# Optimization experiments

Hardware: AMD Instinct MI355X
Metric: run time of the kernel (lower is better)

Reference implementation:

```python
import jax, jax.numpy as jnp
import numpy as np

N_EXPERTS, D_MODEL, D_FF, TOP_K, N_TOKENS = 8, 1024, 4096, 2, 8192

def _uniform_init(key, shape, fan_in):
    # matches torch init: gain = sqrt(1/3), std = gain/sqrt(fan_in), bound = sqrt(3)*std
    bound = np.sqrt(3.0) * np.sqrt(1.0 / 3.0) / np.sqrt(fan_in)
    return jax.random.uniform(key, shape, minval=-bound, maxval=bound, dtype=jnp.float32)

def setup_inputs() -> dict:
    key = jax.random.key(0)
    kx, ki, kw, k1, k2, k3 = jax.random.split(key, 6)
    x = jax.random.normal(kx, (N_TOKENS, D_MODEL), dtype=jnp.float32)
    expert_indices = jax.random.randint(ki, (N_TOKENS, TOP_K), 0, N_EXPERTS, dtype=jnp.int32)
    expert_weights = jax.random.uniform(kw, (N_TOKENS, TOP_K), dtype=jnp.float32)
    w1 = _uniform_init(k1, (N_EXPERTS, D_MODEL, D_FF), D_MODEL)
    w2 = _uniform_init(k2, (N_EXPERTS, D_MODEL, D_FF), D_MODEL)
    w3 = _uniform_init(k3, (N_EXPERTS, D_FF, D_MODEL), D_FF)
    return {"x": x, "expert_indices": expert_indices, "expert_weights": expert_weights,
            "w1": w1, "w2": w2, "w3": w3}

def reference(x, expert_indices, expert_weights, w1, w2, w3):
    # For each token t and routed expert e with routing weight p:
    #   out[t] += p * (silu(x[t] @ W1[e]) * (x[t] @ W2[e])) @ W3[e]
    # Loop over the small fixed expert set; compute each expert's SwiGLU FFN
    # densely over all tokens and combine with per-token routing weights
    # (mathematically identical to the sorted-dispatch grouped GEMM).
    n_experts = w1.shape[0]
    out = jnp.zeros_like(x)
    for e in range(n_experts):
        gate = x @ w1[e]                 # [N, d_ff]
        val = x @ w2[e]                  # [N, d_ff]
        y = (jax.nn.silu(gate) * val) @ w3[e]   # [N, d_model]
        # sum routing weights over top_k slots that picked expert e
        p = jnp.sum(jnp.where(expert_indices == e, expert_weights, 0.0), axis=1)
        out = out + p[:, None] * y
    return out
```

## Files before the change

### kernel.cpp

```cpp
#include <hip/hip_runtime.h>
#include <hip/hip_bf16.h>

typedef __attribute__((ext_vector_type(8))) short short8;
typedef __attribute__((ext_vector_type(4))) float f32x4;
typedef unsigned short u16;
typedef unsigned int u32;

#define NTOK   8192
#define DMODEL 1024
#define DFF    4096
#define NEXP   8
#define NPAIR  (NTOK * 2)
#define PADM   256
#define MT1    72
#define PPAD   (MT1 * PADM)

#define OFF_XB   0ull
#define OFF_W1T  (OFF_XB  + (size_t)NTOK * DMODEL * 2)
#define OFF_W2T  (OFF_W1T + (size_t)NEXP * DFF * DMODEL * 2)
#define OFF_W3T  (OFF_W2T + (size_t)NEXP * DFF * DMODEL * 2)
#define OFF_H    (OFF_W3T + (size_t)NEXP * DMODEL * DFF * 2)
#define OFF_TOK  (OFF_H   + (size_t)PPAD * DFF * 2)
#define OFF_WGT  (OFF_TOK + (size_t)PPAD * 4)
#define OFF_CNT  (OFF_WGT + (size_t)PPAD * 4)
#define OFF_CUR  (OFF_CNT + 64)
#define OFF_OFFP (OFF_CUR + 64)
#define WS_END   (OFF_OFFP + 64)

#define GLOAD16(gp, lp)                                                        \
  __builtin_amdgcn_global_load_lds(                                            \
      (const __attribute__((address_space(1))) u32*)(gp),                      \
      (__attribute__((address_space(3))) u32*)(lp), 16, 0, 0)

__device__ __forceinline__ u16 f2bu(float f) {
  __hip_bfloat16 b = __float2bfloat16(f);
  return __builtin_bit_cast(u16, b);
}


__global__ __launch_bounds__(256) void cvt_x_k(const float* __restrict__ x,
                                               u16* __restrict__ xb) {
  int i = blockIdx.x * 256 + threadIdx.x;
  float4 v = ((const float4*)x)[i];
  unsigned long long pk = (unsigned long long)f2bu(v.x) |
                          ((unsigned long long)f2bu(v.y) << 16) |
                          ((unsigned long long)f2bu(v.z) << 32) |
                          ((unsigned long long)f2bu(v.w) << 48);
  ((unsigned long long*)xb)[i] = pk;
}

__global__ __launch_bounds__(256) void tr_cvt_k(const float* __restrict__ src,
                                                u16* __restrict__ dst, int R, int C) {
  src += (size_t)blockIdx.z * R * C;
  dst += (size_t)blockIdx.z * R * C;
  const int c0 = blockIdx.x * 64, r0 = blockIdx.y * 128;
  __shared__ u16 t[128][68];
  const int tid = threadIdx.x;
  const int cl = (tid & 15) * 4, rl = tid >> 4;
#pragma unroll
  for (int p = 0; p < 8; ++p) {
    int r = rl + p * 16;
    float4 v = *(const float4*)(src + (size_t)(r0 + r) * C + c0 + cl);
    unsigned long long pk = (unsigned long long)f2bu(v.x) |
                            ((unsigned long long)f2bu(v.y) << 16) |
                            ((unsigned long long)f2bu(v.z) << 32) |
                            ((unsigned long long)f2bu(v.w) << 48);
    *(unsigned long long*)&t[r][cl] = pk;
  }
  __syncthreads();
  const int c = tid >> 2, seg = tid & 3;
#pragma unroll
  for (int s = 0; s < 4; ++s) {
    int rbase = (s * 4 + seg) * 8;
    short8 o;
#pragma unroll
    for (int j = 0; j < 8; ++j) o[j] = (short)t[rbase + j][c];
    *(short8*)(dst + (size_t)(c0 + c) * R + r0 + rbase) = o;
  }
}


__global__ __launch_bounds__(256) void count_k(const int* __restrict__ ei,
                                               int* __restrict__ cnt) {
  int i = blockIdx.x * 256 + threadIdx.x;
  atomicAdd(&cnt[ei[i]], 1);
}

__global__ void scan_k(const int* __restrict__ cnt, int* __restrict__ offp) {
  if (threadIdx.x == 0) {
    int a = 0;
#pragma unroll
    for (int e = 0; e < NEXP; ++e) { offp[e] = a; a += (cnt[e] + PADM - 1) & ~(PADM - 1); }
    offp[NEXP] = a;
  }
}

__global__ __launch_bounds__(256) void scatter_k(const int* __restrict__ ei,
                                                 const float* __restrict__ ew,
                                                 const int* __restrict__ offp,
                                                 int* __restrict__ cur,
                                                 int* __restrict__ tok,
                                                 float* __restrict__ wg) {
  int i = blockIdx.x * 256 + threadIdx.x;
  int e = ei[i];
  int p = offp[e] + atomicAdd(&cur[e], 1);
  tok[p] = i >> 1;
  wg[p] = ew[i];
}


#define S1_BUF 16384
#define S1_NK  32

__global__ __launch_bounds__(512, 2) void stage1_k(const u16* __restrict__ xb,
                                                   const u16* __restrict__ w1t,
                                                   const u16* __restrict__ w2t,
                                                   u16* __restrict__ h,
                                                   const int* __restrict__ tok,
                                                   const int* __restrict__ offp) {
  extern __shared__ __align__(16) u16 lds[];
  const int r0 = blockIdx.y * PADM;
  if (r0 >= offp[NEXP]) return;
  int e = 0;
#pragma unroll
  for (int q = 0; q < 7; ++q) e += (offp[e + 1] <= r0) ? 1 : 0;
  const int n0 = blockIdx.x * 128;
  const int tid = threadIdx.x;
  const int lane = tid & 63, w = tid >> 6;
  const int wm = w >> 2, wn = w & 3;

  const int sl = lane & 3, rl = lane >> 2;
  const u16* aga[2];
  int adb[2];
#pragma unroll
  for (int j = 0; j < 2; ++j) {
    int row = w * 32 + j * 16 + rl;
    int t = tok[r0 + row];
    aga[j] = xb + (size_t)t * DMODEL + ((sl ^ ((row >> 1) & 3)) << 3);
    adb[j] = (w * 32 + j * 16) * 32;
  }
  const u16* w1e = w1t + (size_t)e * DFF * DMODEL;
  const u16* w2e = w2t + (size_t)e * DFF * DMODEL;
  const u16* bg1; const u16* bg2;
  int bdb;
  {
    int row = w * 16 + rl;
    size_t ro = (size_t)(n0 + row) * DMODEL + ((sl ^ ((row >> 1) & 3)) << 3);
    bg1 = w1e + ro; bg2 = w2e + ro;
    bdb = (w * 16) * 32;
  }

  int aoff[8], boff[2];
  {
    int ks = lane >> 4;
#pragma unroll
    for (int mi = 0; mi < 8; ++mi) {
      int row = wm * 128 + mi * 16 + (lane & 15);
      aoff[mi] = row * 32 + ((ks ^ ((row >> 1) & 3)) << 3);
    }
#pragma unroll
    for (int ni = 0; ni < 2; ++ni) {
      int col = wn * 32 + ni * 16 + (lane & 15);
      boff[ni] = col * 32 + ((ks ^ ((col >> 1) & 3)) << 3);
    }
  }

  f32x4 accg[8][2], accv[8][2];
  const f32x4 zero = {0.f, 0.f, 0.f, 0.f};
#pragma unroll
  for (int mi = 0; mi < 8; ++mi)
#pragma unroll
    for (int ni = 0; ni < 2; ++ni) { accg[mi][ni] = zero; accv[mi][ni] = zero; }

#define S1_ISSUE(Q, KO)                                                        \
  do {                                                                         \
    GLOAD16(aga[0] + (KO), (Q) + adb[0]);                                      \
    GLOAD16(aga[1] + (KO), (Q) + adb[1]);                                      \
    GLOAD16(bg1 + (KO), (Q) + 8192 + bdb);                                     \
    GLOAD16(bg2 + (KO), (Q) + 12288 + bdb);                                    \
  } while (0)

  S1_ISSUE(lds, 0);
  S1_ISSUE(lds + S1_BUF, 32);
  asm volatile("s_waitcnt vmcnt(4)" ::: "memory");
  __builtin_amdgcn_s_barrier();
  __builtin_amdgcn_sched_barrier(0);

#define S1_STEP(P, KC, ISSUE)                                                  \
  {                                                                            \
    const u16* Ab  = lds + (P) * S1_BUF;                                       \
    const u16* B1b = Ab + 8192;                                                \
    const u16* B2b = Ab + 12288;                                               \
    short8 af[8], b1f[2], b2f[2];                                              \
    _Pragma("unroll") for (int mi = 0; mi < 8; ++mi)                           \
      af[mi] = *(const short8*)(Ab + aoff[mi]);                                \
    _Pragma("unroll") for (int ni = 0; ni < 2; ++ni) {                         \
      b1f[ni] = *(const short8*)(B1b + boff[ni]);                              \
      b2f[ni] = *(const short8*)(B2b + boff[ni]);                              \
    }                                                                          \
    if (ISSUE) S1_ISSUE(lds + (((P) + 2) % 3) * S1_BUF, ((KC) + 2) * 32);      \
    __builtin_amdgcn_s_setprio(1);                                             \
    _Pragma("unroll") for (int mi = 0; mi < 8; ++mi)                           \
      _Pragma("unroll") for (int ni = 0; ni < 2; ++ni) {                       \
        accg[mi][ni] = __builtin_amdgcn_mfma_f32_16x16x32_bf16(                \
            af[mi], b1f[ni], accg[mi][ni], 0, 0, 0);                           \
        accv[mi][ni] = __builtin_amdgcn_mfma_f32_16x16x32_bf16(                \
            af[mi], b2f[ni], accv[mi][ni], 0, 0, 0);                           \
      }                                                                        \
    __builtin_amdgcn_s_setprio(0);                                             \
    if (ISSUE) asm volatile("s_waitcnt vmcnt(4)" ::: "memory");                \
    else       asm volatile("s_waitcnt vmcnt(0)" ::: "memory");                \
    __builtin_amdgcn_s_barrier();                                              \
    __builtin_amdgcn_sched_barrier(0);                                         \
  }

  for (int kc = 0; kc < S1_NK - 2; kc += 3) {
    S1_STEP(0, kc, 1)
    S1_STEP(1, kc + 1, 1)
    S1_STEP(2, kc + 2, 1)
  }
  S1_STEP(0, S1_NK - 2, 0)
  S1_STEP(1, S1_NK - 1, 0)
#undef S1_STEP
#undef S1_ISSUE

  const int prow = r0 + wm * 128 + ((lane >> 4) << 2);
  const int pcol = n0 + wn * 32 + (lane & 15);
#pragma unroll
  for (int mi = 0; mi < 8; ++mi)
#pragma unroll
    for (int ni = 0; ni < 2; ++ni)
#pragma unroll
      for (int j = 0; j < 4; ++j) {
        float g = accg[mi][ni][j];
        float v = accv[mi][ni][j];
        float s = g / (1.f + __expf(-g));
        h[(size_t)(prow + mi * 16 + j) * DFF + (pcol + ni * 16)] = f2bu(s * v);
      }
}


#define S2_BUF 12288
#define S2_NK  128

__global__ __launch_bounds__(512, 4) void stage2_k(const u16* __restrict__ h,
                                                   const u16* __restrict__ w3t,
                                                   float* __restrict__ out,
                                                   const int* __restrict__ tok,
                                                   const float* __restrict__ wg,
                                                   const int* __restrict__ offp) {
  extern __shared__ __align__(16) u16 lds[];
  const int orig = blockIdx.y * 4 + blockIdx.x;
  const int wgid = (orig & 7) * 72 + (orig >> 3);
  const int bx = wgid & 3, by = wgid >> 2;
  const int r0 = by * 128;
  if (r0 >= offp[NEXP]) return;
  int e = 0;
#pragma unroll
  for (int q = 0; q < 7; ++q) e += (offp[e + 1] <= r0) ? 1 : 0;
  const int n0 = bx * 256;
  const int tid = threadIdx.x;
  const int lane = tid & 63, w = tid >> 6;
  const int wm = w >> 2, wn = w & 3;

  const int sl = lane & 3, rl = lane >> 2;
  const u16* aga;
  int adb;
  {
    int row = w * 16 + rl;
    aga = h + (size_t)(r0 + row) * DFF + ((sl ^ ((row >> 1) & 3)) << 3);
    adb = (w * 16) * 32;
  }
  const u16* w3e = w3t + (size_t)e * DMODEL * DFF;
  const u16* bga[2];
  int bdb[2];
#pragma unroll
  for (int j = 0; j < 2; ++j) {
    int row = w * 32 + j * 16 + rl;
    bga[j] = w3e + (size_t)(n0 + row) * DFF + ((sl ^ ((row >> 1) & 3)) << 3);
    bdb[j] = 4096 + (w * 32 + j * 16) * 32;
  }

  int aoff[4], boff[4];
  {
    int ks = lane >> 4;
#pragma unroll
    for (int mi = 0; mi < 4; ++mi) {
      int row = wm * 64 + mi * 16 + (lane & 15);
      aoff[mi] = row * 32 + ((ks ^ ((row >> 1) & 3)) << 3);
    }
#pragma unroll
    for (int ni = 0; ni < 4; ++ni) {
      int col = wn * 64 + ni * 16 + (lane & 15);
      boff[ni] = 4096 + col * 32 + ((ks ^ ((col >> 1) & 3)) << 3);
    }
  }

  f32x4 acc[4][4];
  const f32x4 zero = {0.f, 0.f, 0.f, 0.f};
#pragma unroll
  for (int mi = 0; mi < 4; ++mi)
#pragma unroll
    for (int ni = 0; ni < 4; ++ni) acc[mi][ni] = zero;

#define S2_ISSUE(Q, KO)                                                        \
  do {                                                                         \
    GLOAD16(aga + (KO), (Q) + adb);                                            \
    GLOAD16(bga[0] + (KO), (Q) + bdb[0]);                                      \
    GLOAD16(bga[1] + (KO), (Q) + bdb[1]);                                      \
  } while (0)

  S2_ISSUE(lds, 0);
  S2_ISSUE(lds + S2_BUF, 32);
  asm volatile("s_waitcnt vmcnt(3)" ::: "memory");
  __builtin_amdgcn_s_barrier();
  __builtin_amdgcn_sched_barrier(0);

#define S2_STEP(P, KC, ISSUE)                                                  \
  {                                                                            \
    const u16* Qb = lds + (P) * S2_BUF;                                        \
    short8 af[4], bf[4];                                                       \
    _Pragma("unroll") for (int mi = 0; mi < 4; ++mi)                           \
      af[mi] = *(const short8*)(Qb + aoff[mi]);                                \
    _Pragma("unroll") for (int ni = 0; ni < 4; ++ni)                           \
      bf[ni] = *(const short8*)(Qb + boff[ni]);                                \
    if (ISSUE) S2_ISSUE(lds + (((P) + 2) % 3) * S2_BUF, ((KC) + 2) * 32);      \
    __builtin_amdgcn_s_setprio(1);                                             \
    _Pragma("unroll") for (int mi = 0; mi < 4; ++mi)                           \
      _Pragma("unroll") for (int ni = 0; ni < 4; ++ni)                         \
        acc[mi][ni] = __builtin_amdgcn_mfma_f32_16x16x32_bf16(                 \
            af[mi], bf[ni], acc[mi][ni], 0, 0, 0);                             \
    __builtin_amdgcn_s_setprio(0);                                             \
    if (ISSUE) asm volatile("s_waitcnt vmcnt(3)" ::: "memory");                \
    else       asm volatile("s_waitcnt vmcnt(0)" ::: "memory");                \
    __builtin_amdgcn_s_barrier();                                              \
    __builtin_amdgcn_sched_barrier(0);                                         \
  }

  for (int kc = 0; kc < S2_NK - 2; kc += 3) {
    S2_STEP(0, kc, 1)
    S2_STEP(1, kc + 1, 1)
    S2_STEP(2, kc + 2, 1)
  }
  S2_STEP(0, S2_NK - 2, 0)
  S2_STEP(1, S2_NK - 1, 0)
#undef S2_STEP
#undef S2_ISSUE

  const int prow = r0 + wm * 64 + ((lane >> 4) << 2);
  const int pcolb = n0 + wn * 64 + (lane & 15);
#pragma unroll
  for (int mi = 0; mi < 4; ++mi)
#pragma unroll
    for (int j = 0; j < 4; ++j) {
      int pos = prow + mi * 16 + j;
      float p = wg[pos];
      if (p != 0.f) {
        int t = tok[pos];
#pragma unroll
        for (int ni = 0; ni < 4; ++ni)
          atomicAdd(&out[(size_t)t * DMODEL + pcolb + ni * 16], p * acc[mi][ni][j]);
      }
    }
}


extern "C" void kernel_launch(void* const* d_in, const int* in_sizes, int n_in,
                              void* d_out, int out_size, void* d_ws, size_t ws_size,
                              hipStream_t stream) {
  (void)in_sizes; (void)n_in;
  const float* x  = (const float*)d_in[0];
  const int*   ei = (const int*)d_in[1];
  const float* ew = (const float*)d_in[2];
  const float* w1 = (const float*)d_in[3];
  const float* w2 = (const float*)d_in[4];
  const float* w3 = (const float*)d_in[5];
  float* out = (float*)d_out;
  char* ws = (char*)d_ws;

  hipMemsetAsync(out, 0, (size_t)out_size * sizeof(float), stream);
  if (ws_size < WS_END) return;

  u16* xb   = (u16*)(ws + OFF_XB);
  u16* w1t  = (u16*)(ws + OFF_W1T);
  u16* w2t  = (u16*)(ws + OFF_W2T);
  u16* w3t  = (u16*)(ws + OFF_W3T);
  u16* hb   = (u16*)(ws + OFF_H);
  int* tok  = (int*)(ws + OFF_TOK);
  float* wg = (float*)(ws + OFF_WGT);
  int* cnt  = (int*)(ws + OFF_CNT);
  int* cur  = (int*)(ws + OFF_CUR);
  int* offp = (int*)(ws + OFF_OFFP);

  hipMemsetAsync(ws + OFF_TOK, 0, (size_t)(WS_END - OFF_TOK), stream);

  hipFuncSetAttribute(reinterpret_cast<const void*>(stage1_k),
                      hipFuncAttributeMaxDynamicSharedMemorySize, 98304);
  hipFuncSetAttribute(reinterpret_cast<const void*>(stage2_k),
                      hipFuncAttributeMaxDynamicSharedMemorySize, 73728);

  cvt_x_k<<<dim3(NTOK * DMODEL / 4 / 256), 256, 0, stream>>>(x, xb);
  tr_cvt_k<<<dim3(DFF / 64, DMODEL / 128, NEXP), 256, 0, stream>>>(w1, w1t, DMODEL, DFF);
  tr_cvt_k<<<dim3(DFF / 64, DMODEL / 128, NEXP), 256, 0, stream>>>(w2, w2t, DMODEL, DFF);
  tr_cvt_k<<<dim3(DMODEL / 64, DFF / 128, NEXP), 256, 0, stream>>>(w3, w3t, DFF, DMODEL);
  count_k<<<dim3(NPAIR / 256), 256, 0, stream>>>(ei, cnt);
  scan_k<<<1, 64, 0, stream>>>(cnt, offp);
  scatter_k<<<dim3(NPAIR / 256), 256, 0, stream>>>(ei, ew, offp, cur, tok, wg);
  stage1_k<<<dim3(DFF / 128, MT1), 512, 98304, stream>>>(xb, w1t, w2t, hb, tok, offp);
  stage2_k<<<dim3(DMODEL / 256, PPAD / 128), 512, 73728, stream>>>(hb, w3t, out, tok, wg, offp);
}
```

Baseline: 806.0 us.

## Merge weight conversions into one launch and fuse routing into single-block kernel

Replaces three separate transpose-convert launches with one kernel that covers w1, w2 and w3, using taller 256-row tiles. Count, scan and scatter, plus the workspace memset, are folded into a single 1024-thread block that uses shared-memory counters and wave ballots. This cuts launch count and global atomics. The cost is that routing runs serially on one CU, and the larger LDS tile may lower occupancy of the conversion kernel.

```diff
diff --git a/kernel.cpp b/kernel.cpp
--- a/kernel.cpp
+++ b/kernel.cpp
@@ -22,9 +22,7 @@
 #define OFF_H    (OFF_W3T + (size_t)NEXP * DMODEL * DFF * 2)
 #define OFF_TOK  (OFF_H   + (size_t)PPAD * DFF * 2)
 #define OFF_WGT  (OFF_TOK + (size_t)PPAD * 4)
-#define OFF_CNT  (OFF_WGT + (size_t)PPAD * 4)
-#define OFF_CUR  (OFF_CNT + 64)
-#define OFF_OFFP (OFF_CUR + 64)
+#define OFF_OFFP (OFF_WGT + (size_t)PPAD * 4)
 #define WS_END   (OFF_OFFP + 64)
 
 #define GLOAD16(gp, lp)                                                        \
@@ -49,16 +47,33 @@
   ((unsigned long long*)xb)[i] = pk;
 }
 
-__global__ __launch_bounds__(256) void tr_cvt_k(const float* __restrict__ src,
-                                                u16* __restrict__ dst, int R, int C) {
-  src += (size_t)blockIdx.z * R * C;
-  dst += (size_t)blockIdx.z * R * C;
-  const int c0 = blockIdx.x * 64, r0 = blockIdx.y * 128;
-  __shared__ u16 t[128][68];
+__global__ __launch_bounds__(256) void wcvt_k(const float* __restrict__ w1,
+                                              const float* __restrict__ w2,
+                                              const float* __restrict__ w3,
+                                              u16* __restrict__ w1t,
+                                              u16* __restrict__ w2t,
+                                              u16* __restrict__ w3t) {
+  const int z = blockIdx.y;
+  const float* src; u16* dst; int R, C, tx, ty;
+  if (z < 16) {
+    R = DMODEL; C = DFF;
+    int e = z & 7;
+    src = ((z < 8) ? w1 : w2) + (size_t)e * R * C;
+    dst = ((z < 8) ? w1t : w2t) + (size_t)e * R * C;
+    tx = blockIdx.x & 63; ty = blockIdx.x >> 6;
+  } else {
+    R = DFF; C = DMODEL;
+    int e = z - 16;
+    src = w3 + (size_t)e * R * C;
+    dst = w3t + (size_t)e * R * C;
+    tx = blockIdx.x & 15; ty = blockIdx.x >> 4;
+  }
+  const int c0 = tx * 64, r0 = ty * 256;
+  __shared__ u16 t[256][68];
   const int tid = threadIdx.x;
   const int cl = (tid & 15) * 4, rl = tid >> 4;
 #pragma unroll
-  for (int p = 0; p < 8; ++p) {
+  for (int p = 0; p < 16; ++p) {
     int r = rl + p * 16;
     float4 v = *(const float4*)(src + (size_t)(r0 + r) * C + c0 + cl);
     unsigned long long pk = (unsigned long long)f2bu(v.x) |
@@ -70,8 +85,8 @@
   __syncthreads();
   const int c = tid >> 2, seg = tid & 3;
 #pragma unroll
-  for (int s = 0; s < 4; ++s) {
-    int rbase = (s * 4 + seg) * 8;
+  for (int u = 0; u < 8; ++u) {
+    int rbase = seg * 8 + u * 32;
     short8 o;
 #pragma unroll
     for (int j = 0; j < 8; ++j) o[j] = (short)t[rbase + j][c];
@@ -80,32 +95,39 @@
 }
 
 
-__global__ __launch_bounds__(256) void count_k(const int* __restrict__ ei,
-                                               int* __restrict__ cnt) {
-  int i = blockIdx.x * 256 + threadIdx.x;
-  atomicAdd(&cnt[ei[i]], 1);
-}
-
-__global__ void scan_k(const int* __restrict__ cnt, int* __restrict__ offp) {
-  if (threadIdx.x == 0) {
+__global__ __launch_bounds__(1024) void route_k(const int* __restrict__ ei,
+                                                const float* __restrict__ ew,
+                                                int* __restrict__ tok,
+                                                float* __restrict__ wg,
+                                                int* __restrict__ offp_g) {
+  __shared__ int cnt[NEXP], offp[NEXP + 1], cur[NEXP];
+  const int tid = threadIdx.x;
+  if (tid < NEXP) { cnt[tid] = 0; cur[tid] = 0; }
+  __syncthreads();
+  for (int i = tid; i < PPAD; i += 1024) { tok[i] = 0; wg[i] = 0.f; }
+  for (int i = tid; i < NPAIR; i += 1024) {
+    int e = ei[i];
+#pragma unroll
+    for (int x = 0; x < NEXP; ++x) {
+      unsigned long long m = __ballot(e == x);
+      if ((tid & 63) == 0 && m) atomicAdd(&cnt[x], (int)__popcll(m));
+    }
+  }
+  __syncthreads();
+  if (tid == 0) {
     int a = 0;
 #pragma unroll
     for (int e = 0; e < NEXP; ++e) { offp[e] = a; a += (cnt[e] + PADM - 1) & ~(PADM - 1); }
     offp[NEXP] = a;
   }
-}
-
-__global__ __launch_bounds__(256) void scatter_k(const int* __restrict__ ei,
-                                                 const float* __restrict__ ew,
-                                                 const int* __restrict__ offp,
-                                                 int* __restrict__ cur,
-                                                 int* __restrict__ tok,
-                                                 float* __restrict__ wg) {
-  int i = blockIdx.x * 256 + threadIdx.x;
-  int e = ei[i];
-  int p = offp[e] + atomicAdd(&cur[e], 1);
-  tok[p] = i >> 1;
-  wg[p] = ew[i];
+  __syncthreads();
+  for (int i = tid; i < NPAIR; i += 1024) {
+    int e = ei[i];
+    int p = offp[e] + atomicAdd(&cur[e], 1);
+    tok[p] = i >> 1;
+    wg[p] = ew[i];
+  }
+  if (tid <= NEXP) offp_g[tid] = offp[tid];
 }
 
 
@@ -388,11 +410,7 @@
   u16* hb   = (u16*)(ws + OFF_H);
   int* tok  = (int*)(ws + OFF_TOK);
   float* wg = (float*)(ws + OFF_WGT);
-  int* cnt  = (int*)(ws + OFF_CNT);
-  int* cur  = (int*)(ws + OFF_CUR);
   int* offp = (int*)(ws + OFF_OFFP);
-
-  hipMemsetAsync(ws + OFF_TOK, 0, (size_t)(WS_END - OFF_TOK), stream);
 
   hipFuncSetAttribute(reinterpret_cast<const void*>(stage1_k),
                       hipFuncAttributeMaxDynamicSharedMemorySize, 98304);
@@ -400,12 +418,8 @@
                       hipFuncAttributeMaxDynamicSharedMemorySize, 73728);
 
   cvt_x_k<<<dim3(NTOK * DMODEL / 4 / 256), 256, 0, stream>>>(x, xb);
-  tr_cvt_k<<<dim3(DFF / 64, DMODEL / 128, NEXP), 256, 0, stream>>>(w1, w1t, DMODEL, DFF);
-  tr_cvt_k<<<dim3(DFF / 64, DMODEL / 128, NEXP), 256, 0, stream>>>(w2, w2t, DMODEL, DFF);
-  tr_cvt_k<<<dim3(DMODEL / 64, DFF / 128, NEXP), 256, 0, stream>>>(w3, w3t, DFF, DMODEL);
-  count_k<<<dim3(NPAIR / 256), 256, 0, stream>>>(ei, cnt);
-  scan_k<<<1, 64, 0, stream>>>(cnt, offp);
-  scatter_k<<<dim3(NPAIR / 256), 256, 0, stream>>>(ei, ew, offp, cur, tok, wg);
+  wcvt_k<<<dim3(256, 24), 256, 0, stream>>>(w1, w2, w3, w1t, w2t, w3t);
+  route_k<<<dim3(1), 1024, 0, stream>>>(ei, ew, tok, wg, offp);
   stage1_k<<<dim3(DFF / 128, MT1), 512, 98304, stream>>>(xb, w1t, w2t, hb, tok, offp);
   stage2_k<<<dim3(DMODEL / 256, PPAD / 128), 512, 73728, stream>>>(hb, w3t, out, tok, wg, offp);
 }
```

New measurement: 706.2 us. 12.4% less time.
